# Optimization experiments

Hardware: AMD Instinct MI355X
Metric: run time of the kernel (lower is better)

Reference implementation:

```python
import jax, jax.numpy as jnp
import numpy as np

B, L, S, E, H, Z = 512, 128, 64, 256, 256, 64

def _ln(x, g, b):
    m = jnp.mean(x, -1, keepdims=True)
    v = jnp.mean((x - m) ** 2, -1, keepdims=True)
    return (x - m) / jnp.sqrt(v + 1e-5) * g + b

def _gru_layer(x, Wih, Whh, bih, bhh):
    # x: (B, T, in) -> (outputs (B, T, H), last hidden (B, H)); torch nn.GRU gate math
    xg = jnp.swapaxes(jnp.einsum('bti,gi->btg', x, Wih) + bih, 0, 1)  # (T, B, 3H) precomputed input gates
    h0 = jnp.zeros((x.shape[0], Whh.shape[1]), x.dtype)
    def step(h, xg_t):
        hg = h @ Whh.T + bhh
        xr, xz, xn = jnp.split(xg_t, 3, -1)
        hr, hz, hn = jnp.split(hg, 3, -1)
        r = jax.nn.sigmoid(xr + hr)
        zg = jax.nn.sigmoid(xz + hz)
        n = jnp.tanh(xn + r * hn)
        h_new = (1.0 - zg) * n + zg * h
        return h_new, h_new
    hT, ys = jax.lax.scan(step, h0, xg)
    return jnp.swapaxes(ys, 0, 1), hT

def setup_inputs() -> dict:
    key = jax.random.key(0)
    ks = iter(jax.random.split(key, 64))
    def u(shape, fan):
        s = 1.0 / np.sqrt(fan)
        return jax.random.uniform(next(ks), shape, jnp.float32, -s, s)
    inp = {
        'x': jax.random.normal(next(ks), (B, L, S), jnp.float32),
        'eps': jax.random.normal(next(ks), (B, Z), jnp.float32),
        'dec_noise': jax.random.normal(next(ks), (B, L, Z), jnp.float32),
        'in_W': u((E, S), S), 'in_b': u((E,), S),
        'in_g': jnp.ones((E,), jnp.float32), 'in_beta': jnp.zeros((E,), jnp.float32),
        'eW0i': u((3 * H, E), H), 'eW0h': u((3 * H, H), H), 'eb0i': u((3 * H,), H), 'eb0h': u((3 * H,), H),
        'eW1i': u((3 * H, H), H), 'eW1h': u((3 * H, H), H), 'eb1i': u((3 * H,), H), 'eb1h': u((3 * H,), H),
        'mu_W': u((Z, H), H), 'mu_b': u((Z,), H), 'lv_W': u((Z, H), H), 'lv_b': u((Z,), H),
        'dW0i': u((3 * H, Z), H), 'dW0h': u((3 * H, H), H), 'db0i': u((3 * H,), H), 'db0h': u((3 * H,), H),
        'dW1i': u((3 * H, H), H), 'dW1h': u((3 * H, H), H), 'db1i': u((3 * H,), H), 'db1h': u((3 * H,), H),
        'post_W': u((H, H), H), 'post_b': u((H,), H),
        'post_g': jnp.ones((H,), jnp.float32), 'post_beta': jnp.zeros((H,), jnp.float32),
        'out_W': u((S, H), H), 'out_b': u((S,), H),
    }
    return inp

def reference(x, eps, dec_noise, in_W, in_b, in_g, in_beta,
              eW0i, eW0h, eb0i, eb0h, eW1i, eW1h, eb1i, eb1h,
              mu_W, mu_b, lv_W, lv_b,
              dW0i, dW0h, db0i, db0h, dW1i, dW1h, db1i, db1h,
              post_W, post_b, post_g, post_beta, out_W, out_b):
    # encode
    h = _ln(jax.nn.relu(x @ in_W.T + in_b), in_g, in_beta)          # input_proj
    h, _ = _gru_layer(h, eW0i, eW0h, eb0i, eb0h)                    # encoder GRU layer 0
    _, h_last = _gru_layer(h, eW1i, eW1h, eb1i, eb1h)               # encoder GRU layer 1, h_n[-1]
    mu = h_last @ mu_W.T + mu_b
    log_var = h_last @ lv_W.T + lv_b
    z = mu + eps * jnp.exp(0.5 * log_var)                           # reparameterize
    # decode
    z_seq = jnp.broadcast_to(z[:, None, :], (z.shape[0], L, Z)) + dec_noise * 0.05
    d, _ = _gru_layer(z_seq, dW0i, dW0h, db0i, db0h)
    d, _ = _gru_layer(d, dW1i, dW1h, db1i, db1h)
    d = _ln(jax.nn.relu(d @ post_W.T + post_b), post_g, post_beta)  # post_rnn_proj
    x_hat = jnp.tanh(d @ out_W.T + out_b)                           # output_layer
    return (x_hat, mu, log_var)
```

## Files before the change

### kernel.cpp

```cpp
#include <hip/hip_runtime.h>
#include <hip/hip_bf16.h>
#include <stdint.h>

#define DEVI static __device__ __forceinline__

typedef __bf16 bf16x8 __attribute__((ext_vector_type(8)));
typedef float f32x4 __attribute__((ext_vector_type(4)));
typedef int   int4v __attribute__((ext_vector_type(4)));
typedef int   int2v __attribute__((ext_vector_type(2)));

DEVI float bf2f(uint16_t u){ uint32_t x = ((uint32_t)u) << 16; float f; __builtin_memcpy(&f, &x, 4); return f; }
DEVI uint16_t f2bf(float f){ uint32_t u; __builtin_memcpy(&u, &f, 4); uint32_t r = (u + 0x7FFFu + ((u >> 16) & 1u)) >> 16; return (uint16_t)r; }
DEVI float frcp(float x){ return __builtin_amdgcn_rcpf(x); }
DEVI float sigm(float x){ return frcp(1.f + __expf(-x)); }
DEVI float tanhfast(float x){ return 1.f - 2.f * frcp(1.f + __expf(2.f * x)); }
DEVI f32x4 mfma16(bf16x8 a, bf16x8 b, f32x4 c){ return __builtin_amdgcn_mfma_f32_16x16x32_bf16(a, b, c, 0, 0, 0); }

DEVI bf16x8 cvt8(const float* __restrict__ p){
    f32x4 a = *(const f32x4*)p, b = *(const f32x4*)(p + 4);
    union { bf16x8 v; uint16_t u[8]; } r;
    #pragma unroll
    for (int e = 0; e < 4; ++e) { r.u[e] = f2bf(a[e]); r.u[4 + e] = f2bf(b[e]); }
    return r.v;
}
DEVI int4v asint4(bf16x8 v){ int4v r; __builtin_memcpy(&r, &v, 16); return r; }

DEVI void bar_lds(){
    asm volatile("s_waitcnt lgkmcnt(0)" ::: "memory");
    __builtin_amdgcn_s_barrier();
    __builtin_amdgcn_sched_barrier(0);
}


__global__ __launch_bounds__(256) void k_inproj(
    const float* __restrict__ X, const float* __restrict__ W,
    const float* __restrict__ bias, const float* __restrict__ g,
    const float* __restrict__ beta, uint16_t* __restrict__ Y)
{
    __shared__ __align__(16) char As[64 * 128];
    __shared__ __align__(16) char Bs[256 * 128];
    __shared__ __align__(16) char Cs[64 * 520];
    const int tid = threadIdx.x;
    const long rowbase = (long)blockIdx.x * 64;

    #pragma unroll
    for (int it = 0; it < 2; ++it) {
        int c = it * 256 + tid; int r = c >> 3, cc = c & 7;
        bf16x8 v = cvt8(X + (rowbase + r) * 64 + cc * 8);
        *(int4v*)(As + r * 128 + ((cc * 16) ^ ((r & 7) << 4))) = asint4(v);
    }
    #pragma unroll
    for (int it = 0; it < 8; ++it) {
        int c = it * 256 + tid; int r = c >> 3, cc = c & 7;
        bf16x8 v = cvt8(W + r * 64 + cc * 8);
        *(int4v*)(Bs + r * 128 + ((cc * 16) ^ ((r & 7) << 4))) = asint4(v);
    }
    __syncthreads();

    const int w = tid >> 6, l = tid & 63, lr = l & 15, lg = l >> 4;
    f32x4 acc[16];
    #pragma unroll
    for (int i = 0; i < 16; ++i) acc[i] = (f32x4){0.f, 0.f, 0.f, 0.f};
    const int arow = w * 16 + lr;
    #pragma unroll
    for (int ks = 0; ks < 2; ++ks) {
        bf16x8 a = *(bf16x8*)(As + arow * 128 + ((ks * 64 + lg * 16) ^ ((arow & 7) << 4)));
        #pragma unroll
        for (int tl = 0; tl < 16; ++tl) {
            int n = tl * 16 + lr;
            bf16x8 b = *(bf16x8*)(Bs + n * 128 + ((ks * 64 + lg * 16) ^ ((n & 7) << 4)));
            acc[tl] = mfma16(a, b, acc[tl]);
        }
    }
    float gv[16], bv[16], biasv[16];
    #pragma unroll
    for (int tl = 0; tl < 16; ++tl) {
        int col = tl * 16 + lr;
        gv[tl] = g[col]; bv[tl] = beta[col]; biasv[tl] = bias[col];
    }
    #pragma unroll
    for (int i = 0; i < 4; ++i) {
        float s = 0.f, sq = 0.f, v[16];
        #pragma unroll
        for (int tl = 0; tl < 16; ++tl) {
            float xv = acc[tl][i] + biasv[tl]; xv = fmaxf(xv, 0.f);
            v[tl] = xv; s += xv; sq += xv * xv;
        }
        #pragma unroll
        for (int d = 1; d < 16; d <<= 1) { s += __shfl_xor(s, d); sq += __shfl_xor(sq, d); }
        float mean = s * (1.f / 256.f);
        float var  = sq * (1.f / 256.f) - mean * mean;
        float sc   = rsqrtf(var + 1e-5f);
        int rl = w * 16 + lg * 4 + i;
        #pragma unroll
        for (int tl = 0; tl < 16; ++tl)
            *(uint16_t*)(Cs + rl * 520 + (tl * 16 + lr) * 2) =
                f2bf((v[tl] - mean) * sc * gv[tl] + bv[tl]);
    }
    __syncthreads();
    #pragma unroll
    for (int it = 0; it < 16; ++it) {
        int idx = it * 256 + tid;
        int rl = idx >> 6, ch = idx & 63;
        long rg = rowbase + rl;
        long ri = ((rg & 127) << 9) + (rg >> 7);
        *(int2v*)(Y + ri * 256 + ch * 4) = *(int2v*)(Cs + rl * 520 + ch * 8);
    }
}

template<int KIN, bool ZBUILD>
__global__ __launch_bounds__(512) void k_xg(
    const uint16_t* __restrict__ A, const float* __restrict__ W,
    const float* __restrict__ bias, uint16_t* __restrict__ XG,
    const float* __restrict__ zbuf, const float* __restrict__ noise)
{
    constexpr int KB = KIN * 2;
    constexpr int KS = KIN / 32;
    __shared__ __align__(16) char Bs[192 * KB];
    __shared__ __align__(16) char Cs[128 * 400];
    const int tid = threadIdx.x;
    const int nb = blockIdx.y;

    constexpr int CPR = KIN / 8;
    for (int c = tid; c < 192 * CPR; c += 512) {
        int r = c / CPR, cc = c % CPR;
        bf16x8 v = cvt8(W + (long)(nb * 192 + r) * KIN + cc * 8);
        *(int4v*)(Bs + r * KB + ((cc * 16) ^ ((r & 7) << 4))) = asint4(v);
    }
    __syncthreads();

    const int w = tid >> 6, l = tid & 63, lr = l & 15, lg = l >> 4;
    float bvs[12];
    #pragma unroll
    for (int tl = 0; tl < 12; ++tl) bvs[tl] = bias[nb * 192 + tl * 16 + lr];

    for (int rt = 0; rt < 8; ++rt) {
        const long rowb = (long)blockIdx.x * 1024 + rt * 128;
        const long ria  = rowb + w * 16 + lr;
        bf16x8 a[KS];
        if constexpr (!ZBUILD) {
            #pragma unroll
            for (int ks = 0; ks < KS; ++ks)
                a[ks] = *(const bf16x8*)(A + ria * KIN + ks * 32 + lg * 8);
        } else {
            int b = (int)(ria & 511), t = (int)(ria >> 9);
            #pragma unroll
            for (int ks = 0; ks < KS; ++ks) {
                int k0 = ks * 32 + lg * 8;
                const float* zr = zbuf + b * 64 + k0;
                const float* nr = noise + ((long)b * 128 + t) * 64 + k0;
                f32x4 z0 = *(const f32x4*)zr, z1 = *(const f32x4*)(zr + 4);
                f32x4 n0 = *(const f32x4*)nr, n1 = *(const f32x4*)(nr + 4);
                union { bf16x8 v; uint16_t u[8]; } un;
                #pragma unroll
                for (int e = 0; e < 4; ++e) {
                    un.u[e]     = f2bf(z0[e] + 0.05f * n0[e]);
                    un.u[4 + e] = f2bf(z1[e] + 0.05f * n1[e]);
                }
                a[ks] = un.v;
            }
        }
        f32x4 acc[12];
        #pragma unroll
        for (int i = 0; i < 12; ++i) acc[i] = (f32x4){0.f, 0.f, 0.f, 0.f};
        #pragma unroll
        for (int ks = 0; ks < KS; ++ks) {
            #pragma unroll
            for (int tl = 0; tl < 12; ++tl) {
                int n = tl * 16 + lr;
                bf16x8 b = *(bf16x8*)(Bs + n * KB + ((ks * 64 + lg * 16) ^ ((n & 7) << 4)));
                acc[tl] = mfma16(a[ks], b, acc[tl]);
            }
        }
        #pragma unroll
        for (int tl = 0; tl < 12; ++tl) {
            #pragma unroll
            for (int i = 0; i < 4; ++i)
                *(uint16_t*)(Cs + (w * 16 + lg * 4 + i) * 400 + (tl * 16 + lr) * 2) =
                    f2bf(acc[tl][i] + bvs[tl]);
        }
        __syncthreads();
        #pragma unroll
        for (int it = 0; it < 6; ++it) {
            int idx = it * 512 + tid;
            int row = idx / 24, ch = idx % 24;
            *(int4v*)(XG + (rowb + row) * 768 + nb * 192 + ch * 8) =
                *(int4v*)(Cs + row * 400 + ch * 16);
        }
        __syncthreads();
    }
}

__global__ __launch_bounds__(512) void k_gru(
    const uint16_t* __restrict__ XG, const float* __restrict__ Whh,
    const float* __restrict__ bhh, uint16_t* __restrict__ Y,
    float* __restrict__ hlast)
{
    constexpr int L = 128;
    __shared__ __align__(16) char Abuf[2][2 * 512];
    __shared__ __align__(16) char Wt[768 * 80];
    const int tid = threadIdx.x;
    const int w = tid >> 6, l = tid & 63, lr = l & 15, lg = l >> 4;
    const int rowg0 = blockIdx.x * 2;

    ((uint32_t*)Abuf)[tid] = 0;

    #pragma unroll
    for (int it = 0; it < 6; ++it) {
        int c = it * 512 + tid; int r = c >> 2, cc = c & 3;
        bf16x8 v = cvt8(Whh + (long)r * 256 + 224 + cc * 8);
        *(int4v*)(Wt + r * 80 + cc * 16) = asint4(v);
    }

    int gb[6];
    #pragma unroll
    for (int tl = 0; tl < 6; ++tl) gb[tl] = (tl >> 1) * 256 + w * 32 + (tl & 1) * 16;
    bf16x8 wf[6][7];
    #pragma unroll
    for (int tl = 0; tl < 6; ++tl)
        #pragma unroll
        for (int ks = 0; ks < 7; ++ks)
            wf[tl][ks] = cvt8(Whh + (long)(gb[tl] + lr) * 256 + ks * 32 + lg * 8);

    const int i_  = lg & 1;
    const int sub = (lg >> 1) & 1;
    const int col = w * 32 + sub * 16 + lr;
    const float bR = bhh[col], bZ = bhh[256 + col], bN = bhh[512 + col];
    const long rowl = rowg0 + i_;
    const int wrbyte = i_ * 512 + (((col * 2) & ~15) ^ (i_ << 4)) + ((col * 2) & 15);

    uint16_t xga0 = XG[rowl * 768 + col];
    uint16_t xga1 = XG[rowl * 768 + 256 + col];
    uint16_t xga2 = XG[rowl * 768 + 512 + col];
    float h = 0.f;
    const bool wy = (Y != nullptr);
    __syncthreads();

    for (int t = 0; t < L; ++t) {
        const int p = t & 1;
        f32x4 acc[6];
        #pragma unroll
        for (int i = 0; i < 6; ++i) acc[i] = (f32x4){0.f, 0.f, 0.f, 0.f};
        #pragma unroll
        for (int ks = 0; ks < 8; ++ks) {
            bf16x8 a = *(bf16x8*)(Abuf[p] + (lr & 1) * 512 + ((ks * 64 + lg * 16) ^ ((lr & 1) << 4)));
            if (ks < 7) {
                #pragma unroll
                for (int tl = 0; tl < 6; ++tl) acc[tl] = mfma16(a, wf[tl][ks], acc[tl]);
            } else {
                #pragma unroll
                for (int tl = 0; tl < 6; ++tl) {
                    bf16x8 b = *(bf16x8*)(Wt + (gb[tl] + lr) * 80 + lg * 16);
                    acc[tl] = mfma16(a, b, acc[tl]);
                }
            }
        }
        float pre0, pre1, pre2;
        {
            float a0 = i_ ? acc[0][1] : acc[0][0];
            float a1 = i_ ? acc[1][1] : acc[1][0];
            pre0 = sub ? a1 : a0;
            float b0 = i_ ? acc[2][1] : acc[2][0];
            float b1 = i_ ? acc[3][1] : acc[3][0];
            pre1 = sub ? b1 : b0;
            float c0 = i_ ? acc[4][1] : acc[4][0];
            float c1 = i_ ? acc[5][1] : acc[5][0];
            pre2 = sub ? c1 : c0;
        }
        float xr = bf2f(xga0), xz = bf2f(xga1), xn = bf2f(xga2);
        float R = sigm(xr + pre0 + bR);
        float Z = sigm(xz + pre1 + bZ);
        float N = tanhfast(xn + R * (pre2 + bN));
        h = N + Z * (h - N);
        uint16_t hb = f2bf(h);
        *(uint16_t*)(Abuf[p ^ 1] + wrbyte) = hb;

        if (t + 1 < L) {
            const uint16_t* src = XG + ((long)(t + 1) * 512 + rowl) * 768;
            xga0 = src[col]; xga1 = src[256 + col]; xga2 = src[512 + col];
        }
        if (wy) Y[((long)t * 512 + rowl) * 256 + col] = hb;
        bar_lds();
    }
    if (hlast) hlast[rowl * 256 + col] = h;
}

__global__ __launch_bounds__(256) void k_z(
    const float* __restrict__ hlast, const float* __restrict__ muW,
    const float* __restrict__ mub, const float* __restrict__ lvW,
    const float* __restrict__ lvb, const float* __restrict__ eps,
    float* __restrict__ mu_out, float* __restrict__ lv_out,
    float* __restrict__ zout)
{
    __shared__ float hrow[2][256];
    __shared__ float res[2][128];
    const int tid = threadIdx.x;
    const long row0 = (long)blockIdx.x * 2;
    for (int i = tid; i < 512; i += 256) ((float*)hrow)[i] = hlast[row0 * 256 + i];
    __syncthreads();
    const int lrr = tid >> 7, c = tid & 127;
    const float* Wr = (c < 64 ? muW : lvW) + (long)(c & 63) * 256;
    float acc = (c < 64) ? mub[c] : lvb[c & 63];
    const float* hr = hrow[lrr];
    #pragma unroll 8
    for (int k = 0; k < 256; k += 4) {
        f32x4 wv = *(const f32x4*)(Wr + k);
        #pragma unroll
        for (int e = 0; e < 4; ++e) acc += hr[k + e] * wv[e];
    }
    res[lrr][c] = acc;
    long row = row0 + lrr;
    if (c < 64) mu_out[row * 64 + c] = acc;
    else        lv_out[row * 64 + (c & 63)] = acc;
    __syncthreads();
    if (c < 64) {
        float m = res[lrr][c], lv = res[lrr][64 + c];
        zout[row * 64 + c] = m + eps[row * 64 + c] * __expf(0.5f * lv);
    }
}

__global__ __launch_bounds__(256) void k_post(
    const uint16_t* __restrict__ D1, const float* __restrict__ pW,
    const float* __restrict__ pb, const float* __restrict__ pg,
    const float* __restrict__ pbeta, const float* __restrict__ oW,
    const float* __restrict__ ob, float* __restrict__ xhat)
{
    __shared__ __align__(16) char Bs[256 * 512];
    const int tid = threadIdx.x;
    const long rowbase = (long)blockIdx.x * 64;
    #pragma unroll
    for (int it = 0; it < 32; ++it) {
        int c = it * 256 + tid; int r = c >> 5, cc = c & 31;
        bf16x8 v = cvt8(pW + r * 256 + cc * 8);
        *(int4v*)(Bs + r * 512 + ((cc * 16) ^ ((r & 7) << 4))) = asint4(v);
    }
    __syncthreads();
    const int w = tid >> 6, l = tid & 63, lr = l & 15, lg = l >> 4;
    const long arow = rowbase + w * 16 + lr;
    bf16x8 af[8];
    #pragma unroll
    for (int ks = 0; ks < 8; ++ks) af[ks] = *(const bf16x8*)(D1 + arow * 256 + ks * 32 + lg * 8);
    f32x4 acc[16];
    #pragma unroll
    for (int i = 0; i < 16; ++i) acc[i] = (f32x4){0.f, 0.f, 0.f, 0.f};
    #pragma unroll
    for (int ks = 0; ks < 8; ++ks) {
        #pragma unroll
        for (int tl = 0; tl < 16; ++tl) {
            int n = tl * 16 + lr;
            bf16x8 b = *(bf16x8*)(Bs + n * 512 + ((ks * 64 + lg * 16) ^ ((n & 7) << 4)));
            acc[tl] = mfma16(af[ks], b, acc[tl]);
        }
    }
    float gv[16], bv[16], biasv[16];
    #pragma unroll
    for (int tl = 0; tl < 16; ++tl) {
        int col = tl * 16 + lr;
        gv[tl] = pg[col]; bv[tl] = pbeta[col]; biasv[tl] = pb[col];
    }
    uint16_t dl[16][4];
    #pragma unroll
    for (int i = 0; i < 4; ++i) {
        float s = 0.f, sq = 0.f, v[16];
        #pragma unroll
        for (int tl = 0; tl < 16; ++tl) {
            float xv = acc[tl][i] + biasv[tl]; xv = fmaxf(xv, 0.f);
            v[tl] = xv; s += xv; sq += xv * xv;
        }
        #pragma unroll
        for (int d = 1; d < 16; d <<= 1) { s += __shfl_xor(s, d); sq += __shfl_xor(sq, d); }
        float mean = s * (1.f / 256.f);
        float var  = sq * (1.f / 256.f) - mean * mean;
        float sc   = rsqrtf(var + 1e-5f);
        #pragma unroll
        for (int tl = 0; tl < 16; ++tl)
            dl[tl][i] = f2bf((v[tl] - mean) * sc * gv[tl] + bv[tl]);
    }
    __syncthreads();
    #pragma unroll
    for (int tl = 0; tl < 16; ++tl) {
        int col = tl * 16 + lr;
        #pragma unroll
        for (int i = 0; i < 4; ++i) {
            int row = w * 16 + lg * 4 + i;
            *(uint16_t*)(Bs + row * 512 + (((col * 2) & ~15) ^ ((row & 7) << 4)) + ((col * 2) & 15)) = dl[tl][i];
        }
    }
    __syncthreads();
    const int ar2 = w * 16 + lr;
    f32x4 acc2[4];
    #pragma unroll
    for (int i = 0; i < 4; ++i) acc2[i] = (f32x4){0.f, 0.f, 0.f, 0.f};
    #pragma unroll
    for (int ks = 0; ks < 8; ++ks) {
        bf16x8 a = *(bf16x8*)(Bs + ar2 * 512 + ((ks * 64 + lg * 16) ^ ((ar2 & 7) << 4)));
        #pragma unroll
        for (int tl = 0; tl < 4; ++tl) {
            int n = tl * 16 + lr;
            bf16x8 b = cvt8(oW + n * 256 + ks * 32 + lg * 8);
            acc2[tl] = mfma16(a, b, acc2[tl]);
        }
    }
    #pragma unroll
    for (int tl = 0; tl < 4; ++tl) {
        int col = tl * 16 + lr;
        float bo = ob[col];
        #pragma unroll
        for (int i = 0; i < 4; ++i) {
            long ri = rowbase + w * 16 + lg * 4 + i;
            long b = ri & 511, t = ri >> 9;
            xhat[(b * 128 + t) * 64 + col] = tanhfast(acc2[tl][i] + bo);
        }
    }
}

extern "C" void kernel_launch(void* const* d_in, const int* in_sizes, int n_in,
                              void* d_out, int out_size, void* d_ws, size_t ws_size,
                              hipStream_t stream)
{
    (void)in_sizes; (void)n_in; (void)out_size; (void)ws_size;
    const float* x     = (const float*)d_in[0];
    const float* eps   = (const float*)d_in[1];
    const float* dnz   = (const float*)d_in[2];
    const float* in_W  = (const float*)d_in[3];
    const float* in_b  = (const float*)d_in[4];
    const float* in_g  = (const float*)d_in[5];
    const float* in_be = (const float*)d_in[6];
    const float* eW0i  = (const float*)d_in[7];
    const float* eW0h  = (const float*)d_in[8];
    const float* eb0i  = (const float*)d_in[9];
    const float* eb0h  = (const float*)d_in[10];
    const float* eW1i  = (const float*)d_in[11];
    const float* eW1h  = (const float*)d_in[12];
    const float* eb1i  = (const float*)d_in[13];
    const float* eb1h  = (const float*)d_in[14];
    const float* mu_W  = (const float*)d_in[15];
    const float* mu_b  = (const float*)d_in[16];
    const float* lv_W  = (const float*)d_in[17];
    const float* lv_b  = (const float*)d_in[18];
    const float* dW0i  = (const float*)d_in[19];
    const float* dW0h  = (const float*)d_in[20];
    const float* db0i  = (const float*)d_in[21];
    const float* db0h  = (const float*)d_in[22];
    const float* dW1i  = (const float*)d_in[23];
    const float* dW1h  = (const float*)d_in[24];
    const float* db1i  = (const float*)d_in[25];
    const float* db1h  = (const float*)d_in[26];
    const float* postW = (const float*)d_in[27];
    const float* postb = (const float*)d_in[28];
    const float* postg = (const float*)d_in[29];
    const float* postbe= (const float*)d_in[30];
    const float* outW  = (const float*)d_in[31];
    const float* outb  = (const float*)d_in[32];

    char* ws = (char*)d_ws;
    uint16_t* XG   = (uint16_t*)(ws);
    uint16_t* YA   = (uint16_t*)(ws + 100663296);
    uint16_t* YB   = (uint16_t*)(ws + 134217728);
    float*    hlast= (float*)   (ws + 167772160);
    float*    zbuf = (float*)   (ws + 168296448);

    float* out    = (float*)d_out;
    float* mu_out = out + 4194304;
    float* lv_out = out + 4194304 + 32768;

    dim3 b256(256), b512(512);
    dim3 gxg(64, 4);

    k_inproj<<<1024, b256, 0, stream>>>(x, in_W, in_b, in_g, in_be, YA);
    k_xg<256,false><<<gxg, b512, 0, stream>>>(YA, eW0i, eb0i, XG, nullptr, nullptr);
    k_gru<<<256, b512, 0, stream>>>(XG, eW0h, eb0h, YB, nullptr);
    k_xg<256,false><<<gxg, b512, 0, stream>>>(YB, eW1i, eb1i, XG, nullptr, nullptr);
    k_gru<<<256, b512, 0, stream>>>(XG, eW1h, eb1h, nullptr, hlast);
    k_z<<<256, b256, 0, stream>>>(hlast, mu_W, mu_b, lv_W, lv_b, eps, mu_out, lv_out, zbuf);
    k_xg<64,true><<<gxg, b512, 0, stream>>>(nullptr, dW0i, db0i, XG, zbuf, dnz);
    k_gru<<<256, b512, 0, stream>>>(XG, dW0h, db0h, YA, nullptr);
    k_xg<256,false><<<gxg, b512, 0, stream>>>(YA, dW1i, db1i, XG, nullptr, nullptr);
    k_gru<<<256, b512, 0, stream>>>(XG, dW1h, db1h, YB, nullptr);
    k_post<<<1024, b256, 0, stream>>>(YB, postW, postb, postg, postbe, outW, outb, out);
}
```

Baseline: 981.3 us.

## Keep full Whh slice in registers, prefetch A fragments, raise MFMA priority

The GRU recurrent kernel now holds all 8 k-slices of its recurrent-weight tile in registers, which removes the shared-memory weight buffer and its per-step LDS reads. The A-fragment loads are software-pipelined one k-step ahead, and s_setprio wraps the MFMA loop. The LDS XOR swizzle on the hidden-state buffer changes from bit 4 to bit 6. This raises VGPR pressure (48 bf16x8 weight fragments per lane), which may cause spills at 512 threads, and the swizzle change has to match on both the write and read sides.

```diff
diff --git a/kernel.cpp b/kernel.cpp
--- a/kernel.cpp
+++ b/kernel.cpp
@@ -198,28 +198,20 @@
 {
     constexpr int L = 128;
     __shared__ __align__(16) char Abuf[2][2 * 512];
-    __shared__ __align__(16) char Wt[768 * 80];
     const int tid = threadIdx.x;
     const int w = tid >> 6, l = tid & 63, lr = l & 15, lg = l >> 4;
     const int rowg0 = blockIdx.x * 2;
 
-    ((uint32_t*)Abuf)[tid] = 0;
-
-    #pragma unroll
-    for (int it = 0; it < 6; ++it) {
-        int c = it * 512 + tid; int r = c >> 2, cc = c & 3;
-        bf16x8 v = cvt8(Whh + (long)r * 256 + 224 + cc * 8);
-        *(int4v*)(Wt + r * 80 + cc * 16) = asint4(v);
-    }
+    ((uint32_t*)Abuf)[tid & 511] = 0;
 
     int gb[6];
     #pragma unroll
     for (int tl = 0; tl < 6; ++tl) gb[tl] = (tl >> 1) * 256 + w * 32 + (tl & 1) * 16;
-    bf16x8 wf[6][7];
+    bf16x8 wf[6][8];
     #pragma unroll
     for (int tl = 0; tl < 6; ++tl)
         #pragma unroll
-        for (int ks = 0; ks < 7; ++ks)
+        for (int ks = 0; ks < 8; ++ks)
             wf[tl][ks] = cvt8(Whh + (long)(gb[tl] + lr) * 256 + ks * 32 + lg * 8);
 
     const int i_  = lg & 1;
@@ -227,13 +219,14 @@
     const int col = w * 32 + sub * 16 + lr;
     const float bR = bhh[col], bZ = bhh[256 + col], bN = bhh[512 + col];
     const long rowl = rowg0 + i_;
-    const int wrbyte = i_ * 512 + (((col * 2) & ~15) ^ (i_ << 4)) + ((col * 2) & 15);
+    const int wrbyte = i_ * 512 + ((((col * 2) & ~15) ^ (i_ << 6)) | ((col * 2) & 15));
 
     uint16_t xga0 = XG[rowl * 768 + col];
     uint16_t xga1 = XG[rowl * 768 + 256 + col];
     uint16_t xga2 = XG[rowl * 768 + 512 + col];
     float h = 0.f;
     const bool wy = (Y != nullptr);
+    const int arow = lr & 1;
     __syncthreads();
 
     for (int t = 0; t < L; ++t) {
@@ -241,20 +234,21 @@
         f32x4 acc[6];
         #pragma unroll
         for (int i = 0; i < 6; ++i) acc[i] = (f32x4){0.f, 0.f, 0.f, 0.f};
+
+        const char* ab = Abuf[p];
+        bf16x8 acur = *(bf16x8*)(ab + arow * 512 + ((lg * 16) ^ (arow << 6)));
+        __builtin_amdgcn_s_setprio(1);
         #pragma unroll
         for (int ks = 0; ks < 8; ++ks) {
-            bf16x8 a = *(bf16x8*)(Abuf[p] + (lr & 1) * 512 + ((ks * 64 + lg * 16) ^ ((lr & 1) << 4)));
-            if (ks < 7) {
-                #pragma unroll
-                for (int tl = 0; tl < 6; ++tl) acc[tl] = mfma16(a, wf[tl][ks], acc[tl]);
-            } else {
-                #pragma unroll
-                for (int tl = 0; tl < 6; ++tl) {
-                    bf16x8 b = *(bf16x8*)(Wt + (gb[tl] + lr) * 80 + lg * 16);
-                    acc[tl] = mfma16(a, b, acc[tl]);
-                }
-            }
-        }
+            bf16x8 anx;
+            if (ks < 7)
+                anx = *(bf16x8*)(ab + arow * 512 + (((ks + 1) * 64 + lg * 16) ^ (arow << 6)));
+            #pragma unroll
+            for (int tl = 0; tl < 6; ++tl) acc[tl] = mfma16(acur, wf[tl][ks], acc[tl]);
+            acur = anx;
+        }
+        __builtin_amdgcn_s_setprio(0);
+
         float pre0, pre1, pre2;
         {
             float a0 = i_ ? acc[0][1] : acc[0][0];
```

Result: slower. 1.088 ms (+10.9%).
